# Performance work log

Measured on AMD Instinct MI355X. Metric: run time of the kernel, lower is better.

## Reference

```python
import jax, jax.numpy as jnp
import numpy as np

N_NODES = 50000
N_EDGES = 1_600_000
D_NODE = 64
D_EDGE = 16
HEADS = 4
ATT_F = 16  # features[0] / heads = 64 / 4
LN_EPS = 1e-6


def setup_inputs() -> dict:
    key = jax.random.key(0)
    ks = jax.random.split(key, 9)
    nodes = jax.random.normal(ks[0], (N_NODES, D_NODE), dtype=jnp.float32)
    edges = jax.random.normal(ks[1], (N_EDGES, D_EDGE), dtype=jnp.float32)
    receivers = jax.random.randint(ks[2], (N_EDGES,), 0, N_NODES)
    senders = jax.random.randint(ks[3], (N_EDGES,), 0, N_NODES)
    # he_normal-like scale for W (fan_in = input feature dim)
    W = jax.random.normal(ks[4], (HEADS, ATT_F, D_NODE), dtype=jnp.float32) * np.sqrt(2.0 / D_NODE)
    W_edge = jax.random.normal(ks[5], (HEADS, ATT_F, D_EDGE), dtype=jnp.float32) * np.sqrt(2.0 / D_EDGE)
    # xavier_normal-like scale for a
    a = jax.random.normal(ks[6], (HEADS, 3 * ATT_F), dtype=jnp.float32) * np.sqrt(2.0 / (HEADS + 3 * ATT_F))
    ln_scale = jnp.ones((HEADS * ATT_F,), dtype=jnp.float32)
    ln_bias = jnp.zeros((HEADS * ATT_F,), dtype=jnp.float32)
    return {"nodes": nodes, "edges": edges, "receivers": receivers, "senders": senders,
            "W": W, "W_edge": W_edge, "a": a, "ln_scale": ln_scale, "ln_bias": ln_bias}


def reference(nodes, edges, receivers, senders, W, W_edge, a, ln_scale, ln_bias):
    n = nodes.shape[0]
    # add self edges (zero edge features)
    self_idx = jnp.arange(n)
    r = jnp.concatenate([receivers, self_idx], axis=0)          # [Etot]
    s = jnp.concatenate([senders, self_idx], axis=0)            # [Etot]
    e = jnp.concatenate([edges, jnp.zeros((n, edges.shape[1]), edges.dtype)], axis=0)  # [Etot, De]

    # project node features once, then gather per edge
    Wn = jnp.einsum('hfi,ni->nhf', W, nodes)                    # [N, H, F]
    Ws = Wn[s]                                                   # [Etot, H, F]
    Wr = Wn[r]                                                   # [Etot, H, F]
    We = jnp.einsum('hfi,ei->ehf', W_edge, e)                   # [Etot, H, F]

    # attention logits: a . [Ws || Wr || We], computed without materializing the concat
    a_s, a_r, a_e = jnp.split(a, 3, axis=-1)                    # each [H, F]
    msg = (jnp.einsum('ehf,hf->eh', Ws, a_s)
           + jnp.einsum('ehf,hf->eh', Wr, a_r)
           + jnp.einsum('ehf,hf->eh', We, a_e))                 # [Etot, H]
    lm = jax.nn.leaky_relu(msg)

    # segment softmax over edges grouped by receiver
    seg_max = jax.ops.segment_max(lm, r, num_segments=n)        # [N, H]
    z = lm - seg_max[r]
    exp_z = jnp.exp(z)
    norm = jax.ops.segment_sum(exp_z, r, num_segments=n)        # [N, H]
    alpha = exp_z / norm[r]                                     # [Etot, H]

    # attention-weighted scatter-sum aggregation
    att_msg = alpha[:, :, None] * Ws                            # [Etot, H, F]
    aggr = jax.ops.segment_sum(att_msg, r, num_segments=n)      # [N, H, F]
    out = aggr.reshape(n, -1)                                   # [N, H*F]

    out = jax.nn.elu(out)
    # LayerNorm (flax default: eps=1e-6, scale & bias over last axis)
    mean = jnp.mean(out, axis=-1, keepdims=True)
    var = jnp.mean(jnp.square(out - mean), axis=-1, keepdims=True)
    out = (out - mean) * jax.lax.rsqrt(var + LN_EPS)
    out = out * ln_scale + ln_bias
    return out
```

## Files before the change

### kernel.cpp

```cpp
#include <hip/hip_runtime.h>
#include <hip/hip_fp16.h>

#define LEAKY_SLOPE 0.01f
#define LN_EPS 1e-6f
#define SUBS 8
#define CAP 352
#define MAXE (SUBS*CAP)
#define CSTRIDE 16
#define K3T 512

typedef float  f4v __attribute__((ext_vector_type(4)));

__device__ __forceinline__ float head_sel(int h, float a, float b, float c, float d) {
    float lo = (h & 1) ? b : a;
    float hi = (h & 1) ? d : c;
    return (h & 2) ? hi : lo;
}

__device__ __forceinline__ int xcc_id() {
    return (int)(__builtin_amdgcn_s_getreg(20 | (3 << 11)) & 7);
}

__global__ __launch_bounds__(256) void node_proj_kernel(
    const float* __restrict__ nodes, const float* __restrict__ W,
    const float* __restrict__ a, __half* __restrict__ Wn16,
    float* __restrict__ s_s, float* __restrict__ s_r,
    float* __restrict__ lm_self, int* __restrict__ cursor,
    int ncursor, int N)
{
    int t = threadIdx.x;
    int ci = blockIdx.x * 256 + t;
    if (ci < ncursor) cursor[ci] = 0;

    int lane = t & 63;
    int wv = t >> 6;
    float w[64];
    const float4* W4 = (const float4*)W;
    #pragma unroll
    for (int i = 0; i < 16; i++) {
        float4 v = W4[lane * 16 + i];
        w[4*i] = v.x; w[4*i+1] = v.y; w[4*i+2] = v.z; w[4*i+3] = v.w;
    }
    int h = lane >> 4, f = lane & 15;
    float as_ = a[h * 48 + f];
    float ar_ = a[h * 48 + 16 + f];
    int n0 = blockIdx.x * 16 + wv * 4;
    #pragma unroll
    for (int k = 0; k < 4; k++) {
        int n = n0 + k;
        if (n >= N) break;
        const float4* row4 = (const float4*)(nodes + (size_t)n * 64);
        float acc = 0.f;
        #pragma unroll
        for (int c = 0; c < 16; c++) {
            float4 v = row4[c];
            acc += v.x * w[4*c] + v.y * w[4*c+1] + v.z * w[4*c+2] + v.w * w[4*c+3];
        }
        Wn16[(size_t)n * 64 + lane] = __float2half(acc);
        float ps = acc * as_;
        float pr = acc * ar_;
        #pragma unroll
        for (int off = 1; off < 16; off <<= 1) {
            ps += __shfl_xor(ps, off);
            pr += __shfl_xor(pr, off);
        }
        if (f == 0) {
            s_s[n * 4 + h] = ps;
            s_r[n * 4 + h] = pr;
            float v = ps + pr;
            lm_self[n * 4 + h] = v > 0.f ? v : LEAKY_SLOPE * v;
        }
    }
}

__global__ __launch_bounds__(256) void edge_bin_kernel(
    const float* __restrict__ edges, const int* __restrict__ receivers,
    const int* __restrict__ senders, const float* __restrict__ W_edge,
    const float* __restrict__ a, const float* __restrict__ s_s,
    const float* __restrict__ s_r, int* __restrict__ cursor,
    int4* __restrict__ slab, int E)
{
    __shared__ float be[4][16];
    int t = threadIdx.x;
    int e = blockIdx.x * 256 + t;
    bool act = e < E;
    int r = 0, s = 0;
    if (act) {
        r = __builtin_nontemporal_load(receivers + e);
        s = __builtin_nontemporal_load(senders + e);
    }
    if (t < 64) {
        int h = t >> 4, i = t & 15;
        float sm = 0.f;
        #pragma unroll
        for (int f = 0; f < 16; f++)
            sm += W_edge[(h * 16 + f) * 16 + i] * a[h * 48 + 32 + f];
        be[h][i] = sm;
    }
    __syncthreads();
    if (!act) return;

    int b = r >> 6;
    int cidx = b * SUBS + xcc_id();
    int slot = __hip_atomic_fetch_add(&cursor[cidx * CSTRIDE], 1,
                                      __ATOMIC_RELAXED,
                                      __HIP_MEMORY_SCOPE_WORKGROUP);

    const f4v* ef = (const f4v*)(edges + (size_t)e * 16);
    f4v e0 = __builtin_nontemporal_load(ef);
    f4v e1 = __builtin_nontemporal_load(ef + 1);
    f4v e2 = __builtin_nontemporal_load(ef + 2);
    f4v e3 = __builtin_nontemporal_load(ef + 3);
    float4 ssv = ((const float4*)s_s)[s];
    float4 srv = ((const float4*)s_r)[r];
    float ev[16] = {e0[0], e0[1], e0[2], e0[3], e1[0], e1[1], e1[2], e1[3],
                    e2[0], e2[1], e2[2], e2[3], e3[0], e3[1], e3[2], e3[3]};
    float ssa[4] = {ssv.x, ssv.y, ssv.z, ssv.w};
    float sra[4] = {srv.x, srv.y, srv.z, srv.w};
    float lm[4];
    #pragma unroll
    for (int hh = 0; hh < 4; hh++) {
        float se = 0.f;
        #pragma unroll
        for (int i = 0; i < 16; i++) se += be[hh][i] * ev[i];
        float v = ssa[hh] + sra[hh] + se;
        lm[hh] = v > 0.f ? v : LEAKY_SLOPE * v;
    }
    if (slot < CAP) {
        unsigned packA = (unsigned)__half_as_ushort(__float2half(lm[2])) |
                         ((unsigned)__half_as_ushort(__float2half(lm[3])) << 16);
        unsigned packB = (unsigned)s | ((unsigned)(r & 63) << 16);
        slab[(size_t)cidx * CAP + slot] =
            make_int4(__float_as_int(lm[0]), __float_as_int(lm[1]),
                      (int)packA, (int)packB);
    }
}

__global__ __launch_bounds__(K3T) void bucket_sort_kernel(
    const int* __restrict__ cursor, const int4* __restrict__ slab,
    unsigned short* __restrict__ permG, int2* __restrict__ meta, int N)
{
    __shared__ unsigned char  rl8[MAXE];
    __shared__ unsigned short sl16[MAXE];
    __shared__ unsigned short perm[MAXE];
    __shared__ int cnt64[64];
    __shared__ int off64[64];
    __shared__ int cur64[64];

    int b = blockIdx.x;
    int t = threadIdx.x;
    int nn = min(64, N - b * 64);

    if (t < 64) cnt64[t] = 0;
    __syncthreads();

    int c[SUBS], basearr[SUBS];
    int tot = 0;
    #pragma unroll
    for (int sub = 0; sub < SUBS; sub++) {
        int cc = min(cursor[(b * SUBS + sub) * CSTRIDE], CAP);
        c[sub] = cc; basearr[sub] = tot; tot += cc;
    }

    #pragma unroll
    for (int sub = 0; sub < SUBS; sub++) {
        int cc = c[sub], bs = basearr[sub];
        const int* srcW = (const int*)(slab + (size_t)(b * SUBS + sub) * CAP);
        for (int i = t; i < cc; i += K3T) {
            unsigned w = (unsigned)srcW[i * 4 + 3];
            int rl = (int)((w >> 16) & 63u);
            rl8[bs + i]  = (unsigned char)rl;
            sl16[bs + i] = (unsigned short)(sub * CAP + i);
            atomicAdd(&cnt64[rl], 1);
        }
    }
    __syncthreads();

    if (t < 64) {
        int v = cnt64[t];
        int incl = v;
        #pragma unroll
        for (int off = 1; off < 64; off <<= 1) {
            int u = __shfl_up(incl, off);
            if (t >= off) incl += u;
        }
        off64[t] = incl - v;
        cur64[t] = incl - v;
    }
    __syncthreads();

    for (int i = t; i < tot; i += K3T) {
        int rl = (int)rl8[i];
        int pos = atomicAdd(&cur64[rl], 1);
        perm[pos] = sl16[i];
    }
    __syncthreads();

    unsigned short* pg = permG + (size_t)b * MAXE;
    for (int pos = t; pos < tot; pos += K3T)
        pg[pos] = perm[pos];

    if (t < nn)
        meta[b * 64 + t] = make_int2(b * MAXE + off64[t], cnt64[t]);
}

__global__ __launch_bounds__(256) void node_aggr_kernel(
    const __half* __restrict__ Wn16, const float* __restrict__ lm_self,
    const int2* __restrict__ meta, const int4* __restrict__ slab,
    const unsigned short* __restrict__ permG,
    const float* __restrict__ ln_scale, const float* __restrict__ ln_bias,
    float* __restrict__ out, int N)
{
    __shared__ float lds_w[4][64][4];
    __shared__ int   lds_s[4][64];
    int t = threadIdx.x;
    int lane = t & 63;
    int wv = t >> 6;
    int n = blockIdx.x * 4 + wv;
    if (n >= N) return;
    int2 mt = meta[n];
    int beg = mt.x, cntn = mt.y;
    int h = lane >> 4;
    const int4* slabB = slab + (size_t)(n >> 6) * MAXE;

    float acc = 0.f, acc2 = 0.f;
    float p0 = 0.f, p1 = 0.f, p2 = 0.f, p3 = 0.f;

    for (int base = 0; base < cntn; base += 64) {
        int j = base + lane;
        float w0 = 0.f, w1 = 0.f, w2 = 0.f, w3 = 0.f;
        int sv = 0;
        if (j < cntn) {
            int slot = (int)permG[beg + j];
            int4 pl = slabB[slot];
            w0 = __expf(__int_as_float(pl.x));
            w1 = __expf(__int_as_float(pl.y));
            unsigned pa = (unsigned)pl.z;
            w2 = __expf(__half2float(__ushort_as_half((unsigned short)(pa & 0xFFFFu))));
            w3 = __expf(__half2float(__ushort_as_half((unsigned short)(pa >> 16))));
            sv = (int)((unsigned)pl.w & 0xFFFFu);
        }
        p0 += w0; p1 += w1; p2 += w2; p3 += w3;
        lds_s[wv][lane] = sv;
        *(float4*)&lds_w[wv][lane][0] = make_float4(w0, w1, w2, w3);
        int cnt = min(64, cntn - base);
        int k = 0;
        for (; k + 1 < cnt; k += 2) {
            int   sk0 = lds_s[wv][k];
            int   sk1 = lds_s[wv][k + 1];
            float a0  = lds_w[wv][k][h];
            float a1  = lds_w[wv][k + 1][h];
            acc  += a0 * __half2float(Wn16[(size_t)sk0 * 64 + lane]);
            acc2 += a1 * __half2float(Wn16[(size_t)sk1 * 64 + lane]);
        }
        if (k < cnt)
            acc += lds_w[wv][k][h] * __half2float(Wn16[(size_t)lds_s[wv][k] * 64 + lane]);
    }
    acc += acc2;

    #pragma unroll
    for (int off = 1; off < 64; off <<= 1) {
        p0 += __shfl_xor(p0, off);
        p1 += __shfl_xor(p1, off);
        p2 += __shfl_xor(p2, off);
        p3 += __shfl_xor(p3, off);
    }
    float4 ls = ((const float4*)lm_self)[n];
    float ws0 = __expf(ls.x), ws1 = __expf(ls.y);
    float ws2 = __expf(ls.z), ws3 = __expf(ls.w);
    float totd  = head_sel(h, p0 + ws0, p1 + ws1, p2 + ws2, p3 + ws3);
    float wself = head_sel(h, ws0, ws1, ws2, ws3);
    acc = (acc + wself * __half2float(Wn16[(size_t)n * 64 + lane])) / totd;

    float y = acc > 0.f ? acc : expm1f(acc);
    float sum = y;
    #pragma unroll
    for (int off = 1; off < 64; off <<= 1) sum += __shfl_xor(sum, off);
    float mean = sum * 0.015625f;
    float d = y - mean;
    float vs = d * d;
    #pragma unroll
    for (int off = 1; off < 64; off <<= 1) vs += __shfl_xor(vs, off);
    float var = vs * 0.015625f;
    float o = d * rsqrtf(var + LN_EPS) * ln_scale[lane] + ln_bias[lane];
    out[(size_t)n * 64 + lane] = o;
}

extern "C" void kernel_launch(void* const* d_in, const int* in_sizes, int n_in,
                              void* d_out, int out_size, void* d_ws, size_t ws_size,
                              hipStream_t stream) {
    const float* nodes     = (const float*)d_in[0];
    const float* edges     = (const float*)d_in[1];
    const int*   receivers = (const int*)d_in[2];
    const int*   senders   = (const int*)d_in[3];
    const float* W         = (const float*)d_in[4];
    const float* W_edge    = (const float*)d_in[5];
    const float* a         = (const float*)d_in[6];
    const float* ln_scale  = (const float*)d_in[7];
    const float* ln_bias   = (const float*)d_in[8];
    float* out = (float*)d_out;

    int N = in_sizes[0] / 64;
    int E = in_sizes[2];
    int NB = (N + 63) / 64;
    int ncursor = NB * SUBS * CSTRIDE;

    char* ws = (char*)d_ws;
    size_t off = 0;
    auto alloc = [&](size_t bytes) -> void* {
        void* p = ws + off;
        off += (bytes + 15) & ~(size_t)15;
        return p;
    };
    __half* Wn16   = (__half*)alloc((size_t)N * 64 * 2);
    float* s_s     = (float*)alloc((size_t)N * 4 * 4);
    float* s_r     = (float*)alloc((size_t)N * 4 * 4);
    float* lm_self = (float*)alloc((size_t)N * 4 * 4);
    int*   cursor  = (int*)alloc((size_t)ncursor * 4);
    int2*  meta    = (int2*)alloc((size_t)N * 8);
    unsigned short* permG = (unsigned short*)alloc((size_t)NB * MAXE * 2);
    int4*  slab    = (int4*)alloc((size_t)NB * MAXE * 16);
    (void)ws_size; (void)n_in; (void)out_size;

    node_proj_kernel<<<(N + 15) / 16, 256, 0, stream>>>(
        nodes, W, a, Wn16, s_s, s_r, lm_self, cursor, ncursor, N);
    edge_bin_kernel<<<(E + 255) / 256, 256, 0, stream>>>(
        edges, receivers, senders, W_edge, a, s_s, s_r, cursor, slab, E);
    bucket_sort_kernel<<<NB, K3T, 0, stream>>>(cursor, slab, permG, meta, N);
    node_aggr_kernel<<<(N + 3) / 4, 256, 0, stream>>>(
        Wn16, lm_self, meta, slab, permG, ln_scale, ln_bias, out, N);
}
```

Baseline: 384.4 us.

## Fuse bucket sort and node aggregation into one LDS-resident kernel

Merges the per-bucket sort and the per-node aggregation into one kernel. The sorted edge records are kept as full int4 payloads in shared memory, so the global permutation array and meta array are no longer written and re-read. Each wave now handles 16 nodes serially, with 4-way unrolled gathers and the softmax denominator computed per head inline. The trade-off is fewer blocks (one per 64 nodes, about 45KB LDS each), which cuts occupancy and parallelism for the gather-heavy aggregation phase.

```diff
diff --git a/kernel.cpp b/kernel.cpp
--- a/kernel.cpp
+++ b/kernel.cpp
@@ -7,7 +7,6 @@
 #define CAP 352
 #define MAXE (SUBS*CAP)
 #define CSTRIDE 16
-#define K3T 512
 
 typedef float  f4v __attribute__((ext_vector_type(4)));
 
@@ -15,6 +14,13 @@
     float lo = (h & 1) ? b : a;
     float hi = (h & 1) ? d : c;
     return (h & 2) ? hi : lo;
+}
+
+__device__ __forceinline__ float unpack_lm(int h, int4 p) {
+    unsigned pa = (unsigned)p.z;
+    float lm2 = __half2float(__ushort_as_half((unsigned short)(pa & 0xFFFFu)));
+    float lm3 = __half2float(__ushort_as_half((unsigned short)(pa >> 16)));
+    return head_sel(h, __int_as_float(p.x), __int_as_float(p.y), lm2, lm3);
 }
 
 __device__ __forceinline__ int xcc_id() {
@@ -136,43 +142,33 @@
     }
 }
 
-__global__ __launch_bounds__(K3T) void bucket_sort_kernel(
+__global__ __launch_bounds__(256) void sort_aggr_kernel(
+    const __half* __restrict__ Wn16, const float* __restrict__ lm_self,
     const int* __restrict__ cursor, const int4* __restrict__ slab,
-    unsigned short* __restrict__ permG, int2* __restrict__ meta, int N)
+    const float* __restrict__ ln_scale, const float* __restrict__ ln_bias,
+    float* __restrict__ out, int N)
 {
-    __shared__ unsigned char  rl8[MAXE];
-    __shared__ unsigned short sl16[MAXE];
-    __shared__ unsigned short perm[MAXE];
+    __shared__ int4 raw[MAXE];
     __shared__ int cnt64[64];
     __shared__ int off64[64];
     __shared__ int cur64[64];
 
     int b = blockIdx.x;
     int t = threadIdx.x;
-    int nn = min(64, N - b * 64);
 
     if (t < 64) cnt64[t] = 0;
     __syncthreads();
 
-    int c[SUBS], basearr[SUBS];
-    int tot = 0;
+    int c[SUBS];
+    #pragma unroll
+    for (int sub = 0; sub < SUBS; sub++)
+        c[sub] = min(cursor[(b * SUBS + sub) * CSTRIDE], CAP);
+
     #pragma unroll
     for (int sub = 0; sub < SUBS; sub++) {
-        int cc = min(cursor[(b * SUBS + sub) * CSTRIDE], CAP);
-        c[sub] = cc; basearr[sub] = tot; tot += cc;
-    }
-
-    #pragma unroll
-    for (int sub = 0; sub < SUBS; sub++) {
-        int cc = c[sub], bs = basearr[sub];
         const int* srcW = (const int*)(slab + (size_t)(b * SUBS + sub) * CAP);
-        for (int i = t; i < cc; i += K3T) {
-            unsigned w = (unsigned)srcW[i * 4 + 3];
-            int rl = (int)((w >> 16) & 63u);
-            rl8[bs + i]  = (unsigned char)rl;
-            sl16[bs + i] = (unsigned short)(sub * CAP + i);
-            atomicAdd(&cnt64[rl], 1);
-        }
+        for (int i = t; i < c[sub]; i += 256)
+            atomicAdd(&cnt64[((unsigned)srcW[i * 4 + 3] >> 16) & 63], 1);
     }
     __syncthreads();
 
@@ -189,101 +185,75 @@
     }
     __syncthreads();
 
-    for (int i = t; i < tot; i += K3T) {
-        int rl = (int)rl8[i];
-        int pos = atomicAdd(&cur64[rl], 1);
-        perm[pos] = sl16[i];
-    }
-    __syncthreads();
-
-    unsigned short* pg = permG + (size_t)b * MAXE;
-    for (int pos = t; pos < tot; pos += K3T)
-        pg[pos] = perm[pos];
-
-    if (t < nn)
-        meta[b * 64 + t] = make_int2(b * MAXE + off64[t], cnt64[t]);
-}
-
-__global__ __launch_bounds__(256) void node_aggr_kernel(
-    const __half* __restrict__ Wn16, const float* __restrict__ lm_self,
-    const int2* __restrict__ meta, const int4* __restrict__ slab,
-    const unsigned short* __restrict__ permG,
-    const float* __restrict__ ln_scale, const float* __restrict__ ln_bias,
-    float* __restrict__ out, int N)
-{
-    __shared__ float lds_w[4][64][4];
-    __shared__ int   lds_s[4][64];
-    int t = threadIdx.x;
+    #pragma unroll
+    for (int sub = 0; sub < SUBS; sub++) {
+        const int4* src = slab + (size_t)(b * SUBS + sub) * CAP;
+        for (int i = t; i < c[sub]; i += 256) {
+            int4 p = src[i];
+            int rl = (int)(((unsigned)p.w >> 16) & 63u);
+            int pos = atomicAdd(&cur64[rl], 1);
+            raw[pos] = p;
+        }
+    }
+    __syncthreads();
+
     int lane = t & 63;
     int wv = t >> 6;
-    int n = blockIdx.x * 4 + wv;
-    if (n >= N) return;
-    int2 mt = meta[n];
-    int beg = mt.x, cntn = mt.y;
     int h = lane >> 4;
-    const int4* slabB = slab + (size_t)(n >> 6) * MAXE;
-
-    float acc = 0.f, acc2 = 0.f;
-    float p0 = 0.f, p1 = 0.f, p2 = 0.f, p3 = 0.f;
-
-    for (int base = 0; base < cntn; base += 64) {
-        int j = base + lane;
-        float w0 = 0.f, w1 = 0.f, w2 = 0.f, w3 = 0.f;
-        int sv = 0;
-        if (j < cntn) {
-            int slot = (int)permG[beg + j];
-            int4 pl = slabB[slot];
-            w0 = __expf(__int_as_float(pl.x));
-            w1 = __expf(__int_as_float(pl.y));
-            unsigned pa = (unsigned)pl.z;
-            w2 = __expf(__half2float(__ushort_as_half((unsigned short)(pa & 0xFFFFu))));
-            w3 = __expf(__half2float(__ushort_as_half((unsigned short)(pa >> 16))));
-            sv = (int)((unsigned)pl.w & 0xFFFFu);
-        }
-        p0 += w0; p1 += w1; p2 += w2; p3 += w3;
-        lds_s[wv][lane] = sv;
-        *(float4*)&lds_w[wv][lane][0] = make_float4(w0, w1, w2, w3);
-        int cnt = min(64, cntn - base);
-        int k = 0;
-        for (; k + 1 < cnt; k += 2) {
-            int   sk0 = lds_s[wv][k];
-            int   sk1 = lds_s[wv][k + 1];
-            float a0  = lds_w[wv][k][h];
-            float a1  = lds_w[wv][k + 1][h];
-            acc  += a0 * __half2float(Wn16[(size_t)sk0 * 64 + lane]);
-            acc2 += a1 * __half2float(Wn16[(size_t)sk1 * 64 + lane]);
-        }
-        if (k < cnt)
-            acc += lds_w[wv][k][h] * __half2float(Wn16[(size_t)lds_s[wv][k] * 64 + lane]);
-    }
-    acc += acc2;
-
-    #pragma unroll
-    for (int off = 1; off < 64; off <<= 1) {
-        p0 += __shfl_xor(p0, off);
-        p1 += __shfl_xor(p1, off);
-        p2 += __shfl_xor(p2, off);
-        p3 += __shfl_xor(p3, off);
-    }
-    float4 ls = ((const float4*)lm_self)[n];
-    float ws0 = __expf(ls.x), ws1 = __expf(ls.y);
-    float ws2 = __expf(ls.z), ws3 = __expf(ls.w);
-    float totd  = head_sel(h, p0 + ws0, p1 + ws1, p2 + ws2, p3 + ws3);
-    float wself = head_sel(h, ws0, ws1, ws2, ws3);
-    acc = (acc + wself * __half2float(Wn16[(size_t)n * 64 + lane])) / totd;
-
-    float y = acc > 0.f ? acc : expm1f(acc);
-    float sum = y;
-    #pragma unroll
-    for (int off = 1; off < 64; off <<= 1) sum += __shfl_xor(sum, off);
-    float mean = sum * 0.015625f;
-    float d = y - mean;
-    float vs = d * d;
-    #pragma unroll
-    for (int off = 1; off < 64; off <<= 1) vs += __shfl_xor(vs, off);
-    float var = vs * 0.015625f;
-    float o = d * rsqrtf(var + LN_EPS) * ln_scale[lane] + ln_bias[lane];
-    out[(size_t)n * 64 + lane] = o;
+
+    for (int k = 0; k < 16; k++) {
+        int nloc = wv * 16 + k;
+        int n = b * 64 + nloc;
+        if (n >= N) break;
+        int cnt = cnt64[nloc];
+        int off = off64[nloc];
+        float a0 = 0.f, a1 = 0.f, a2 = 0.f, a3 = 0.f;
+        float d0 = 0.f, d1 = 0.f, d2 = 0.f, d3 = 0.f;
+        int j = 0;
+        for (; j + 3 < cnt; j += 4) {
+            int4 pA = raw[off + j];
+            int4 pB = raw[off + j + 1];
+            int4 pC = raw[off + j + 2];
+            int4 pD = raw[off + j + 3];
+            float wA = __expf(unpack_lm(h, pA));
+            float wB = __expf(unpack_lm(h, pB));
+            float wC = __expf(unpack_lm(h, pC));
+            float wD = __expf(unpack_lm(h, pD));
+            int sA = (int)((unsigned)pA.w & 0xFFFFu);
+            int sB = (int)((unsigned)pB.w & 0xFFFFu);
+            int sC = (int)((unsigned)pC.w & 0xFFFFu);
+            int sD = (int)((unsigned)pD.w & 0xFFFFu);
+            a0 += wA * __half2float(Wn16[(size_t)sA * 64 + lane]); d0 += wA;
+            a1 += wB * __half2float(Wn16[(size_t)sB * 64 + lane]); d1 += wB;
+            a2 += wC * __half2float(Wn16[(size_t)sC * 64 + lane]); d2 += wC;
+            a3 += wD * __half2float(Wn16[(size_t)sD * 64 + lane]); d3 += wD;
+        }
+        for (; j < cnt; j++) {
+            int4 pA = raw[off + j];
+            float wA = __expf(unpack_lm(h, pA));
+            int sA = (int)((unsigned)pA.w & 0xFFFFu);
+            a0 += wA * __half2float(Wn16[(size_t)sA * 64 + lane]); d0 += wA;
+        }
+        float acc = (a0 + a1) + (a2 + a3);
+        float den = (d0 + d1) + (d2 + d3);
+
+        float4 ls = ((const float4*)lm_self)[n];
+        float wself = __expf(head_sel(h, ls.x, ls.y, ls.z, ls.w));
+        acc = (acc + wself * __half2float(Wn16[(size_t)n * 64 + lane])) / (den + wself);
+
+        float y = acc > 0.f ? acc : expm1f(acc);
+        float sum = y;
+        #pragma unroll
+        for (int o2 = 1; o2 < 64; o2 <<= 1) sum += __shfl_xor(sum, o2);
+        float mean = sum * 0.015625f;
+        float d = y - mean;
+        float vs = d * d;
+        #pragma unroll
+        for (int o2 = 1; o2 < 64; o2 <<= 1) vs += __shfl_xor(vs, o2);
+        float var = vs * 0.015625f;
+        float o = d * rsqrtf(var + LN_EPS) * ln_scale[lane] + ln_bias[lane];
+        out[(size_t)n * 64 + lane] = o;
+    }
 }
 
 extern "C" void kernel_launch(void* const* d_in, const int* in_sizes, int n_in,
@@ -317,8 +287,6 @@
     float* s_r     = (float*)alloc((size_t)N * 4 * 4);
     float* lm_self = (float*)alloc((size_t)N * 4 * 4);
     int*   cursor  = (int*)alloc((size_t)ncursor * 4);
-    int2*  meta    = (int2*)alloc((size_t)N * 8);
-    unsigned short* permG = (unsigned short*)alloc((size_t)NB * MAXE * 2);
     int4*  slab    = (int4*)alloc((size_t)NB * MAXE * 16);
     (void)ws_size; (void)n_in; (void)out_size;
 
@@ -326,7 +294,6 @@
         nodes, W, a, Wn16, s_s, s_r, lm_self, cursor, ncursor, N);
     edge_bin_kernel<<<(E + 255) / 256, 256, 0, stream>>>(
         edges, receivers, senders, W_edge, a, s_s, s_r, cursor, slab, E);
-    bucket_sort_kernel<<<NB, K3T, 0, stream>>>(cursor, slab, permG, meta, N);
-    node_aggr_kernel<<<(N + 3) / 4, 256, 0, stream>>>(
-        Wn16, lm_self, meta, slab, permG, ln_scale, ln_bias, out, N);
-}
+    sort_aggr_kernel<<<NB, 256, 0, stream>>>(
+        Wn16, lm_self, cursor, slab, ln_scale, ln_bias, out, N);
+}
```

Result: slower. 452.9 us (+17.8%).
